# Optimization experiments

Hardware: AMD Instinct MI355X
Metric: run time of the kernel (lower is better)

## Reference

```python
import jax, jax.numpy as jnp
import numpy as np
import math

MARGIN = 0.5
SCALE = 64.0
CURVATURE = 1.0
COS_M = math.cos(MARGIN)
SIN_M = math.sin(MARGIN)
TH = math.cos(math.pi - MARGIN)
MM = math.sin(math.pi - MARGIN) * MARGIN

B, D, C = 2048, 512, 16384


def setup_inputs() -> dict:
    key = jax.random.key(0)
    k1, k2, k3 = jax.random.split(key, 3)
    embeddings = jax.random.normal(k1, (B, D), dtype=jnp.float32) * 0.05  # roughly inside the ball
    labels = jax.random.randint(k2, (B,), 0, C)
    # xavier_uniform for [C, D]
    limit = math.sqrt(6.0 / (C + D))
    weight = jax.random.uniform(k3, (C, D), dtype=jnp.float32, minval=-limit, maxval=limit)
    return {"embeddings": embeddings, "labels": labels, "weight": weight}


def _exp_map_zero(v, c):
    sqrt_c = c ** 0.5
    v_norm = jnp.maximum(jnp.linalg.norm(v, axis=-1, keepdims=True), 1e-7)
    return jnp.tanh(sqrt_c * v_norm) * v / (sqrt_c * v_norm)


def reference(embeddings, labels, weight):
    c = CURVATURE
    # class prototypes mapped onto the Poincare ball, clipped to radius 0.95
    proto = _exp_map_zero(weight, c)                                  # [C, D]
    proto_norm = jnp.linalg.norm(proto, axis=-1, keepdims=True)
    proto = jnp.where(proto_norm > 0.95, proto * 0.95 / proto_norm, proto)

    x = embeddings                                                     # [B, D]
    x_sq = jnp.sum(x * x, axis=-1)                                    # [B]
    y_sq = jnp.sum(proto * proto, axis=-1)                            # [C]
    xy = x @ proto.T                                                  # [B, C]
    diff_sq = jnp.maximum(x_sq[:, None] + y_sq[None, :] - 2.0 * xy, 0.0)

    x_sq_c = jnp.minimum(x_sq, 1.0 - 1e-5)
    y_sq_c = jnp.minimum(y_sq, 1.0 - 1e-5)
    denom = (1.0 - c * x_sq_c)[:, None] * (1.0 - c * y_sq_c)[None, :]
    arg = 1.0 + 2.0 * c * diff_sq / jnp.maximum(denom, 1e-7)
    dists = jnp.arccosh(jnp.maximum(arg, 1.0 + 1e-7)) / (c ** 0.5)    # [B, C]

    sims = jnp.exp(-dists)
    cosine = jnp.clip(2.0 * sims - 1.0, -1.0, 1.0)
    sine = jnp.sqrt(jnp.maximum(1.0 - cosine * cosine, 1e-7))
    phi = cosine * COS_M - sine * SIN_M
    phi = jnp.where(cosine > TH, phi, cosine - MM)

    one_hot = jax.nn.one_hot(labels, cosine.shape[1], dtype=cosine.dtype)
    logits = (one_hot * phi + (1.0 - one_hot) * cosine) * SCALE        # [B, C]

    logp = jax.nn.log_softmax(logits, axis=-1)
    loss = -jnp.mean(jnp.take_along_axis(logp, labels[:, None], axis=1))
    return loss
```

## Files before the change

kernel.cpp:

```cpp
#include <hip/hip_runtime.h>
#include <math.h>

#define Bn 2048
#define Dn 512
#define Cn 16384

typedef float v4f __attribute__((ext_vector_type(4)));

#define WAIT_VM4()  asm volatile("s_waitcnt vmcnt(4)" ::: "memory")
#define WAIT_VM0()  asm volatile("s_waitcnt vmcnt(0)" ::: "memory")
#define RAW_BAR()   asm volatile("s_barrier" ::: "memory")
#define LGKM0_BAR() asm volatile("s_waitcnt lgkmcnt(0)\n\ts_barrier" ::: "memory")

__device__ __forceinline__ void async16(const void* g, void* l) {
  __builtin_amdgcn_global_load_lds(
      (const __attribute__((address_space(1))) char*)g,
      (__attribute__((address_space(3))) char*)l, 16, 0, 0);
}


__device__ __forceinline__ void prep_load(
    int row, int lane, const float* __restrict__ w, const float* __restrict__ x,
    float4& a, float4& b)
{
  const float* src = (row < Cn) ? (w + (size_t)row * Dn) : (x + (size_t)(row - Cn) * Dn);
  const float4* s4 = (const float4*)src;
  a = s4[lane * 2];
  b = s4[lane * 2 + 1];
}

__device__ __forceinline__ void prep_row_vals(
    int row, int lane, float4 a, float4 b,
    char* __restrict__ wq8, char* __restrict__ xq8,
    float* __restrict__ fscale, float* __restrict__ ysqA, float* __restrict__ yrA,
    float* __restrict__ xsA, float* __restrict__ xrA)
{
  bool isW = row < Cn;
  float ss = a.x * a.x + a.y * a.y + a.z * a.z + a.w * a.w
           + b.x * b.x + b.y * b.y + b.z * b.z + b.w * b.w;
  #pragma unroll
  for (int d = 1; d < 64; d <<= 1) ss += __shfl_xor(ss, d);

  int w0 = __builtin_amdgcn_cvt_pk_fp8_f32(a.x * 16.f, a.y * 16.f, 0, false);
  w0     = __builtin_amdgcn_cvt_pk_fp8_f32(a.z * 16.f, a.w * 16.f, w0, true);
  int w1 = __builtin_amdgcn_cvt_pk_fp8_f32(b.x * 16.f, b.y * 16.f, 0, false);
  w1     = __builtin_amdgcn_cvt_pk_fp8_f32(b.z * 16.f, b.w * 16.f, w1, true);
  char* dst = isW ? (wq8 + (size_t)row * Dn) : (xq8 + (size_t)(row - Cn) * Dn);
  ((int2*)dst)[lane] = make_int2(w0, w1);

  if (lane == 0) {
    if (isW) {
      float n = fmaxf(sqrtf(ss), 1e-7f);
      float e2 = __expf(2.f * fminf(n, 10.f));
      float t = (e2 - 1.f) * __builtin_amdgcn_rcpf(e2 + 1.f);
      float tc = fminf(t, 0.95f);
      fscale[row] = tc / n;
      float ys = tc * tc;
      ysqA[row] = ys;
      yrA[row] = 1.f / (1.f - fminf(ys, 1.f - 1e-5f));
    } else {
      int r = row - Cn;
      xsA[r] = ss;
      xrA[r] = 1.f / (1.f - fminf(ss, 1.f - 1e-5f));
    }
  }
}

__device__ __forceinline__ void gemm_job(
    int job, int tid, char* lds,
    const char* __restrict__ xq8, const char* __restrict__ wq8,
    const float* __restrict__ fscale, const float* __restrict__ ysqA,
    const float* __restrict__ yrA, const float* __restrict__ xsA,
    const float* __restrict__ xrA, float* __restrict__ partials)
{
  const int xcd = job & 7;
  const int loc = job >> 3;
  const int mt  = loc & 15;
  const int nt  = (xcd << 4) | (loc >> 4);
  const int mBase = mt * 128;
  const int nBase = nt * 128;
  const int lane = tid & 63;
  const int wv = tid >> 6;
  const int quad = lane >> 4;
  const int l16 = lane & 15;
  const int waveM = wv >> 1;
  const int waveN = wv & 1;

  v4f acc[4][4];
  #pragma unroll
  for (int i = 0; i < 4; ++i)
    #pragma unroll
    for (int j = 0; j < 4; ++j)
      acc[i][j] = (v4f){0.f, 0.f, 0.f, 0.f};

  const int s0 = tid, s1 = tid + 256;
  const int r0 = s0 >> 2, c0 = (s0 & 3) ^ ((r0 >> 1) & 3);
  const int r1 = s1 >> 2, c1 = (s1 & 3) ^ ((r1 >> 1) & 3);
  const char* gA0 = xq8 + (size_t)(mBase + r0) * Dn + c0 * 16;
  const char* gA1 = xq8 + (size_t)(mBase + r1) * Dn + c1 * 16;
  const char* gW0 = wq8 + (size_t)(nBase + r0) * Dn + c0 * 16;
  const char* gW1 = wq8 + (size_t)(nBase + r1) * Dn + c1 * 16;
  const int lo0 = s0 * 16, lo1 = s1 * 16;

  const int kx = (l16 >> 1) & 3;
  int aoff[2], boff[2];
  #pragma unroll
  for (int s = 0; s < 2; ++s) {
    int chunk = (2 * s + (quad >> 1)) ^ kx;
    aoff[s] = (waveM * 64 + l16) * 64 + chunk * 16 + (quad & 1) * 8;
    boff[s] = (waveN * 64 + l16) * 64 + chunk * 16 + (quad & 1) * 8;
  }

  #pragma unroll
  for (int t = 0; t < 2; ++t) {
    char* Ab = lds + t * 16384;
    char* Wb = Ab + 8192;
    async16(gA0 + t * 64, Ab + lo0);
    async16(gA1 + t * 64, Ab + lo1);
    async16(gW0 + t * 64, Wb + lo0);
    async16(gW1 + t * 64, Wb + lo1);
  }

  #pragma unroll
  for (int kt = 0; kt < 8; ++kt) {
    const int cur = kt & 1;
    if (kt < 7) { WAIT_VM4(); } else { WAIT_VM0(); }
    RAW_BAR();
    char* Ab = lds + cur * 16384;
    char* Wb = Ab + 8192;
    long af[4][2], bf[4][2];
    #pragma unroll
    for (int s = 0; s < 2; ++s) {
      #pragma unroll
      for (int i = 0; i < 4; ++i) af[i][s] = *(const long*)(Ab + aoff[s] + i * 1024);
      #pragma unroll
      for (int j = 0; j < 4; ++j) bf[j][s] = *(const long*)(Wb + boff[s] + j * 1024);
    }
    #pragma unroll
    for (int s = 0; s < 2; ++s)
      #pragma unroll
      for (int i = 0; i < 4; ++i)
        #pragma unroll
        for (int j = 0; j < 4; ++j)
          acc[i][j] = __builtin_amdgcn_mfma_f32_16x16x32_fp8_fp8(af[i][s], bf[j][s], acc[i][j], 0, 0, 0);
    LGKM0_BAR();
    if (kt + 2 < 8) {
      async16(gA0 + (kt + 2) * 64, Ab + lo0);
      async16(gA1 + (kt + 2) * 64, Ab + lo1);
      async16(gW0 + (kt + 2) * 64, Wb + lo0);
      async16(gW1 + (kt + 2) * 64, Wb + lo1);
    }
  }

  float ysqj[4], yrj[4], gj[4];
  #pragma unroll
  for (int j = 0; j < 4; ++j) {
    int col = nBase + waveN * 64 + j * 16 + l16;
    gj[j] = -2.f * fscale[col] * (1.f / 256.f);
    ysqj[j] = ysqA[col];
    yrj[j] = yrA[col];
  }
  #pragma unroll
  for (int i = 0; i < 4; ++i) {
    #pragma unroll
    for (int r = 0; r < 4; ++r) {
      int row = mBase + waveM * 64 + i * 16 + quad * 4 + r;
      float xs = xsA[row];
      float xr2 = 2.f * xrA[row];
      float partial = 0.f;
      if (xs >= 0.99999f) {
        #pragma unroll
        for (int j = 0; j < 4; ++j) {
          float d = fmaxf(fmaf(gj[j], acc[i][j][r], xs + ysqj[j]), 0.f);
          float z = fmaf(d, xr2 * yrj[j], 1.f);
          float u = 64.f * __builtin_amdgcn_rcpf(z);
          partial += fmaf(u, fmaf(0.5f, u, 1.f), 1.f);
        }
      } else {
        #pragma unroll
        for (int j = 0; j < 4; ++j) {
          float d = fmaxf(fmaf(gj[j], acc[i][j][r], xs + ysqj[j]), 0.f);
          float z = fmaf(d, xr2 * yrj[j], 1.f);
          float sq = sqrtf(fmaf(z, z, -1.f));
          float u = 128.f * __builtin_amdgcn_rcpf(z + sq);
          partial += __expf(u);
        }
      }
      partial += __shfl_xor(partial, 1);
      partial += __shfl_xor(partial, 2);
      partial += __shfl_xor(partial, 4);
      partial += __shfl_xor(partial, 8);
      if (l16 == 0) partials[(size_t)row * 256 + nt * 2 + waveN] = partial;
    }
  }
}


__global__ __launch_bounds__(256) void prep_kernel(
    const float* __restrict__ w, const float* __restrict__ x,
    char* __restrict__ wq8, char* __restrict__ xq8,
    float* __restrict__ fscale, float* __restrict__ ysqA, float* __restrict__ yrA,
    float* __restrict__ xsA, float* __restrict__ xrA, float* __restrict__ out)
{
  if (blockIdx.x == 0 && threadIdx.x == 0) *out = 0.f;
  const int lane = threadIdx.x & 63;
  const int base = (blockIdx.x * 4 + (threadIdx.x >> 6)) * 4;
  float4 a[4], b[4];
  #pragma unroll
  for (int i = 0; i < 4; ++i) prep_load(base + i, lane, w, x, a[i], b[i]);
  #pragma unroll
  for (int i = 0; i < 4; ++i)
    prep_row_vals(base + i, lane, a[i], b[i], wq8, xq8, fscale, ysqA, yrA, xsA, xrA);
}

__global__ __launch_bounds__(256, 3) void gemm_kernel(
    const char* __restrict__ xq8, const char* __restrict__ wq8,
    const float* __restrict__ fscale, const float* __restrict__ ysqA,
    const float* __restrict__ yrA, const float* __restrict__ xsA,
    const float* __restrict__ xrA, float* __restrict__ partials)
{
  __shared__ int4 ldsv[2048];
  gemm_job(blockIdx.x, threadIdx.x, (char*)ldsv, xq8, wq8, fscale, ysqA, yrA, xsA, xrA, partials);
}

__global__ __launch_bounds__(256) void final_kernel(
    const float* __restrict__ x, const float* __restrict__ w,
    const int* __restrict__ labels, const float* __restrict__ fscale,
    const float* __restrict__ ysqA, const float* __restrict__ yrA,
    const float* __restrict__ xsA, const float* __restrict__ xrA,
    const float* __restrict__ partials, float* __restrict__ out)
{
  const int lane = threadIdx.x & 63;
  const int wvid = threadIdx.x >> 6;
  const int r0 = (blockIdx.x * 4 + wvid) * 2;
  const int r1 = r0 + 1;

  const int lab0 = labels[r0], lab1 = labels[r1];
  const float* pr0 = partials + (size_t)r0 * 256;
  const float* pr1 = partials + (size_t)r1 * 256;
  float sum0 = pr0[lane] + pr0[lane + 64] + pr0[lane + 128] + pr0[lane + 192];
  float sum1 = pr1[lane] + pr1[lane + 64] + pr1[lane + 128] + pr1[lane + 192];

  const float4* xv0 = (const float4*)(x + (size_t)r0 * Dn);
  const float4* xv1 = (const float4*)(x + (size_t)r1 * Dn);
  const float4* wv0 = (const float4*)(w + (size_t)lab0 * Dn);
  const float4* wv1 = (const float4*)(w + (size_t)lab1 * Dn);
  float4 a00 = xv0[lane * 2], a01 = xv0[lane * 2 + 1];
  float4 b00 = wv0[lane * 2], b01 = wv0[lane * 2 + 1];
  float4 a10 = xv1[lane * 2], a11 = xv1[lane * 2 + 1];
  float4 b10 = wv1[lane * 2], b11 = wv1[lane * 2 + 1];
  float dot0 = a00.x * b00.x + a00.y * b00.y + a00.z * b00.z + a00.w * b00.w
             + a01.x * b01.x + a01.y * b01.y + a01.z * b01.z + a01.w * b01.w;
  float dot1 = a10.x * b10.x + a10.y * b10.y + a10.z * b10.z + a10.w * b10.w
             + a11.x * b11.x + a11.y * b11.y + a11.z * b11.z + a11.w * b11.w;

  #pragma unroll
  for (int d = 1; d < 64; d <<= 1) {
    sum0 += __shfl_xor(sum0, d);
    dot0 += __shfl_xor(dot0, d);
    sum1 += __shfl_xor(sum1, d);
    dot1 += __shfl_xor(dot1, d);
  }

  float term = 0.f;
  if (lane == 0) {
    #pragma unroll
    for (int h = 0; h < 2; ++h) {
      const int row = h ? r1 : r0;
      const int lab = h ? lab1 : lab0;
      const float sum = h ? sum1 : sum0;
      const float dot = h ? dot1 : dot0;
      float xy = fscale[lab] * dot;
      float diff = fmaxf(xsA[row] + ysqA[lab] - 2.f * xy, 0.f);
      float z = fmaf(2.f * diff, xrA[row] * yrA[lab], 1.f);
      float sq = sqrtf(fmaf(z, z, -1.f));
      float sims = 1.f / (z + sq);
      float u_lab = 128.f * sims;
      float cosv = fmaf(2.f, sims, -1.f);
      float sine = sqrtf(fmaxf(fmaf(-cosv, cosv, 1.f), 1e-7f));
      float phi = (cosv > -0.8775825619f)
                      ? (cosv * 0.8775825619f - sine * 0.4794255386f)
                      : (cosv - 0.2397127693f);
      float e_lab = __expf(u_lab);
      float e_phi = __expf(fminf(64.f * phi + 64.f, 80.f));
      term += logf(sum - e_lab + e_phi) - 64.f * phi - 64.f;
    }
  }

  __shared__ float red[4];
  if (lane == 0) red[wvid] = term;
  __syncthreads();
  if (threadIdx.x == 0)
    atomicAdd(out, (red[0] + red[1] + red[2] + red[3]) * (1.f / (float)Bn));
}

extern "C" void kernel_launch(void* const* d_in, const int* in_sizes, int n_in,
                              void* d_out, int out_size, void* d_ws, size_t ws_size,
                              hipStream_t stream) {
  (void)in_sizes; (void)n_in; (void)out_size; (void)ws_size;
  const float* emb = (const float*)d_in[0];
  const int* labels = (const int*)d_in[1];
  const float* weight = (const float*)d_in[2];
  float* out = (float*)d_out;

  char* p = (char*)d_ws;
  char* wq8 = p; p += (size_t)Cn * Dn;
  char* xq8 = p; p += (size_t)Bn * Dn;
  float* fscale = (float*)p; p += (size_t)Cn * 4;
  float* ysqA  = (float*)p; p += (size_t)Cn * 4;
  float* yrA   = (float*)p; p += (size_t)Cn * 4;
  float* xsA   = (float*)p; p += (size_t)Bn * 4;
  float* xrA   = (float*)p; p += (size_t)Bn * 4;
  float* partials = (float*)p; p += (size_t)Bn * 256 * 4;

  prep_kernel<<<(Cn + Bn) / 16, 256, 0, stream>>>(weight, emb, wq8, xq8, fscale, ysqA, yrA, xsA, xrA, out);
  gemm_kernel<<<(Bn / 128) * (Cn / 128), 256, 0, stream>>>(
      xq8, wq8, fscale, ysqA, yrA, xsA, xrA, partials);
  final_kernel<<<Bn / 8, 256, 0, stream>>>(emb, weight, labels, fscale, ysqA, yrA, xsA, xrA, partials, out);
}
```

Baseline: 124.4 us.

## Load FP8 GEMM fragments directly from global into registers, dropping LDS staging

The fp8 MFMA GEMM no longer stages tiles through LDS with async global-to-LDS copies and barriers. Each wave now loads its A and B fragments straight from global memory into registers, double-buffered in registers across k-steps. This removes the LDS traffic and block-wide synchronisation, but each tile is fetched by several waves and uses 8-byte non-coalesced loads, relying on L1/L2 for reuse.

```diff
diff --git a/kernel.cpp b/kernel.cpp
--- a/kernel.cpp
+++ b/kernel.cpp
@@ -6,17 +6,6 @@
 #define Cn 16384
 
 typedef float v4f __attribute__((ext_vector_type(4)));
-
-#define WAIT_VM4()  asm volatile("s_waitcnt vmcnt(4)" ::: "memory")
-#define WAIT_VM0()  asm volatile("s_waitcnt vmcnt(0)" ::: "memory")
-#define RAW_BAR()   asm volatile("s_barrier" ::: "memory")
-#define LGKM0_BAR() asm volatile("s_waitcnt lgkmcnt(0)\n\ts_barrier" ::: "memory")
-
-__device__ __forceinline__ void async16(const void* g, void* l) {
-  __builtin_amdgcn_global_load_lds(
-      (const __attribute__((address_space(1))) char*)g,
-      (__attribute__((address_space(3))) char*)l, 16, 0, 0);
-}
 
 
 __device__ __forceinline__ void prep_load(
@@ -67,7 +56,7 @@
 }
 
 __device__ __forceinline__ void gemm_job(
-    int job, int tid, char* lds,
+    int job, int tid,
     const char* __restrict__ xq8, const char* __restrict__ wq8,
     const float* __restrict__ fscale, const float* __restrict__ ysqA,
     const float* __restrict__ yrA, const float* __restrict__ xsA,
@@ -93,48 +82,34 @@
     for (int j = 0; j < 4; ++j)
       acc[i][j] = (v4f){0.f, 0.f, 0.f, 0.f};
 
-  const int s0 = tid, s1 = tid + 256;
-  const int r0 = s0 >> 2, c0 = (s0 & 3) ^ ((r0 >> 1) & 3);
-  const int r1 = s1 >> 2, c1 = (s1 & 3) ^ ((r1 >> 1) & 3);
-  const char* gA0 = xq8 + (size_t)(mBase + r0) * Dn + c0 * 16;
-  const char* gA1 = xq8 + (size_t)(mBase + r1) * Dn + c1 * 16;
-  const char* gW0 = wq8 + (size_t)(nBase + r0) * Dn + c0 * 16;
-  const char* gW1 = wq8 + (size_t)(nBase + r1) * Dn + c1 * 16;
-  const int lo0 = s0 * 16, lo1 = s1 * 16;
-
-  const int kx = (l16 >> 1) & 3;
-  int aoff[2], boff[2];
-  #pragma unroll
-  for (int s = 0; s < 2; ++s) {
-    int chunk = (2 * s + (quad >> 1)) ^ kx;
-    aoff[s] = (waveM * 64 + l16) * 64 + chunk * 16 + (quad & 1) * 8;
-    boff[s] = (waveN * 64 + l16) * 64 + chunk * 16 + (quad & 1) * 8;
-  }
-
-  #pragma unroll
-  for (int t = 0; t < 2; ++t) {
-    char* Ab = lds + t * 16384;
-    char* Wb = Ab + 8192;
-    async16(gA0 + t * 64, Ab + lo0);
-    async16(gA1 + t * 64, Ab + lo1);
-    async16(gW0 + t * 64, Wb + lo0);
-    async16(gW1 + t * 64, Wb + lo1);
-  }
+  unsigned offA[4], offB[4];
+  #pragma unroll
+  for (int i = 0; i < 4; ++i) {
+    offA[i] = (unsigned)((mBase + waveM * 64 + i * 16 + l16) * Dn + quad * 8);
+    offB[i] = (unsigned)((nBase + waveN * 64 + i * 16 + l16) * Dn + quad * 8);
+  }
+
+  long a[2][4][2], b[2][4][2];
+  #pragma unroll
+  for (int i = 0; i < 4; ++i)
+    #pragma unroll
+    for (int s = 0; s < 2; ++s) {
+      a[0][i][s] = *(const long*)(xq8 + offA[i] + s * 32);
+      b[0][i][s] = *(const long*)(wq8 + offB[i] + s * 32);
+    }
 
   #pragma unroll
   for (int kt = 0; kt < 8; ++kt) {
     const int cur = kt & 1;
-    if (kt < 7) { WAIT_VM4(); } else { WAIT_VM0(); }
-    RAW_BAR();
-    char* Ab = lds + cur * 16384;
-    char* Wb = Ab + 8192;
-    long af[4][2], bf[4][2];
-    #pragma unroll
-    for (int s = 0; s < 2; ++s) {
+    const int nxt = cur ^ 1;
+    if (kt < 7) {
       #pragma unroll
-      for (int i = 0; i < 4; ++i) af[i][s] = *(const long*)(Ab + aoff[s] + i * 1024);
-      #pragma unroll
-      for (int j = 0; j < 4; ++j) bf[j][s] = *(const long*)(Wb + boff[s] + j * 1024);
+      for (int i = 0; i < 4; ++i)
+        #pragma unroll
+        for (int s = 0; s < 2; ++s) {
+          a[nxt][i][s] = *(const long*)(xq8 + offA[i] + (kt + 1) * 64 + s * 32);
+          b[nxt][i][s] = *(const long*)(wq8 + offB[i] + (kt + 1) * 64 + s * 32);
+        }
     }
     #pragma unroll
     for (int s = 0; s < 2; ++s)
@@ -142,14 +117,8 @@
       for (int i = 0; i < 4; ++i)
         #pragma unroll
         for (int j = 0; j < 4; ++j)
-          acc[i][j] = __builtin_amdgcn_mfma_f32_16x16x32_fp8_fp8(af[i][s], bf[j][s], acc[i][j], 0, 0, 0);
-    LGKM0_BAR();
-    if (kt + 2 < 8) {
-      async16(gA0 + (kt + 2) * 64, Ab + lo0);
-      async16(gA1 + (kt + 2) * 64, Ab + lo1);
-      async16(gW0 + (kt + 2) * 64, Wb + lo0);
-      async16(gW1 + (kt + 2) * 64, Wb + lo1);
-    }
+          acc[i][j] = __builtin_amdgcn_mfma_f32_16x16x32_fp8_fp8(
+              a[cur][i][s], b[cur][j][s], acc[i][j], 0, 0, 0);
   }
 
   float ysqj[4], yrj[4], gj[4];
@@ -219,8 +188,7 @@
     const float* __restrict__ yrA, const float* __restrict__ xsA,
     const float* __restrict__ xrA, float* __restrict__ partials)
 {
-  __shared__ int4 ldsv[2048];
-  gemm_job(blockIdx.x, threadIdx.x, (char*)ldsv, xq8, wq8, fscale, ysqA, yrA, xsA, xrA, partials);
+  gemm_job(blockIdx.x, threadIdx.x, xq8, wq8, fscale, ysqA, yrA, xsA, xrA, partials);
 }
 
 __global__ __launch_bounds__(256) void final_kernel(
```

After: 212.1 us. 1.71x slower.
